# Kernel optimization log

Hardware: AMD Instinct MI355X
Metric: run time of the kernel (lower is better)

## Reference

```python
import jax, jax.numpy as jnp
import numpy as np

SIZE = 64            # size
DIST = 4             # distance (4x4x4 unshared window)
PAD = DIST // 2      # 2
DS = SIZE - 4        # depth of voxel grid (60)
CONVEY = 0.9
RATE = 5
FC_IN = DS * SIZE * SIZE  # (size-4)*size*size = 245760


def setup_inputs() -> dict:
    key = jax.random.key(0)
    ks = jax.random.split(key, 8)
    vinput = jax.random.normal(ks[0], (DS, SIZE, SIZE, 4), dtype=jnp.float32)
    # location-specific (unshared) 4x4x4 synapse weights per voxel
    synapse = jax.random.normal(ks[1], (DS, SIZE, SIZE, DIST, DIST, DIST), dtype=jnp.float32)
    W1 = jax.random.normal(ks[2], (1024, FC_IN), dtype=jnp.float32) / np.float32(np.sqrt(FC_IN))
    b1 = jnp.zeros((1024,), jnp.float32)
    W2 = jax.random.normal(ks[3], (128, 1024), dtype=jnp.float32) / np.float32(np.sqrt(1024))
    b2 = jnp.zeros((128,), jnp.float32)
    W3 = jax.random.normal(ks[4], (10, 128), dtype=jnp.float32) / np.float32(np.sqrt(128))
    b3 = jnp.zeros((10,), jnp.float32)
    return {"vinput": vinput, "synapse": synapse, "W1": W1, "b1": b1,
            "W2": W2, "b2": b2, "W3": W3, "b3": b3}


def _forward(vinput, synapse, W1, b1, W2, b2, W3, b3):
    # frame is zeros, so neuron_matrix = pad(vinput) on the 3 spatial dims
    nm = jnp.pad(vinput, ((PAD, PAD), (PAD, PAD), (PAD, PAD), (0, 0)))  # (DS+2P, S+2P, S+2P, 4)
    ofs = jnp.arange(DIST)
    # gather indices for the 4x4x4 windows anchored at the top-left (as in the source)
    wi = (jnp.arange(DS)[:, None] + ofs)[:, None, None, :, None, None]
    wj = (jnp.arange(SIZE)[:, None] + ofs)[None, :, None, None, :, None]
    wk = (jnp.arange(SIZE)[:, None] + ofs)[None, None, :, None, None, :]
    for _ in range(RATE):
        # synapse (d,d,d) broadcasts over channel, so the full sum factors
        # through the channel-sum of the neuron matrix.
        ns = nm.sum(-1)                       # (DS+2P, S+2P, S+2P)
        win = ns[wi, wj, wk]                  # (DS, S, S, d, d, d)
        core = jnp.einsum('ijkabc,ijkabc->ijk', synapse, win)  # (DS, S, S)
        # dummy is written only at [0:DS, 0:S, 0:S]; border stays zero.
        nm = jnp.zeros_like(nm).at[:DS, :SIZE, :SIZE, :].set(
            (jax.nn.relu(core) * CONVEY)[..., None])
    x = nm[PAD:DS + PAD, PAD:SIZE + PAD, PAD:SIZE + PAD, :]  # (DS, S, S, 4)
    x = x.reshape(-1, FC_IN)                                 # (4, FC_IN), row-major like torch view
    x = jax.nn.relu(x @ W1.T + b1)
    x = jax.nn.relu(x @ W2.T + b2)
    return x @ W3.T + b3                                     # (4, 10)


def reference(vinput, synapse, W1, b1, W2, b2, W3, b3):
    return _forward(vinput, synapse, W1, b1, W2, b2, W3, b3)
```

## Files before the change

### kernel.cpp

```cpp
#include <hip/hip_runtime.h>

#define DSX 60
#define SZ  64
#define NPT (DSX*SZ*SZ)
#define NS_P 64
#define NS_Q 68
#define NS_R 68
#define NS_SZ (NS_P*NS_Q*NS_R)
#define P_PER_ROW 61440
#define KSPLIT 4
#define P_CHUNK (P_PER_ROW / KSPLIT)
#define PB_SLAB (15*NS_Q*NS_R)

typedef float fx4 __attribute__((ext_vector_type(4)));

__global__ __launch_bounds__(256) void fill_pb(const float* __restrict__ vin,
                                               float* __restrict__ PB0,
                                               float* __restrict__ PB1) {
    int t = blockIdx.x * 256 + threadIdx.x;
    if (t >= NS_SZ) return;
    int r = t % NS_R;
    int q = (t / NS_R) % NS_Q;
    int p = t / (NS_R * NS_Q);
    float val = 0.f;
    if (p >= 2 && p < 62 && q >= 2 && q < 66 && r >= 2 && r < 66) {
        const float* b = vin + ((((size_t)(p - 2) * SZ) + (q - 2)) * SZ + (r - 2)) * 4;
        val = (b[0] + b[1]) + (b[2] + b[3]);
    }
    PB0[t] = val;
    PB1[t] = 0.f;
}

__global__ __launch_bounds__(256) void conv_kernel(const float* __restrict__ PBin,
                                                   const float* __restrict__ syn,
                                                   float* __restrict__ PBout) {
    int t = blockIdx.x * 256 + threadIdx.x;
    if (t >= NPT) return;
    int k = t & 63;
    int j = (t >> 6) & 63;
    int i = t >> 12;
    const float4* s4 = (const float4*)syn + (size_t)t * 16;
    float acc = 0.f;
#pragma unroll
    for (int a = 0; a < 4; a++) {
#pragma unroll
        for (int b = 0; b < 4; b++) {
            float4 w = s4[a * 4 + b];
            const float* nrow = PBin + ((size_t)(i + a) * NS_Q + (j + b)) * NS_R + k;
            acc += w.x * nrow[0] + w.y * nrow[1] + w.z * nrow[2] + w.w * nrow[3];
        }
    }
    PBout[((size_t)i * NS_Q + j) * NS_R + k] = acc > 0.f ? acc * 3.6f : 0.f;
}

__global__ __launch_bounds__(256) void gemv1(const float* __restrict__ W1,
                                             const float* __restrict__ PB,
                                             float* __restrict__ partial) {
    int n = blockIdx.x >> 2;
    int c = blockIdx.x & 3;
    const fx4* w4 = (const fx4*)(W1 + (size_t)n * (P_PER_ROW * 4));
    float a0 = 0.f, a1 = 0.f, a2 = 0.f, a3 = 0.f;
#pragma unroll 4
    for (int it = 0; it < P_CHUNK / 256; it++) {
        int p = c * P_CHUNK + it * 256 + threadIdx.x;
        fx4 w = __builtin_nontemporal_load(&w4[p]);
        float s = (w.x + w.y) + (w.z + w.w);
        int iloc = p >> 12;
        int j = (p >> 6) & 63;
        int k = p & 63;
        int base = ((iloc + 2) * NS_Q + (j + 2)) * NS_R + (k + 2);
        a0 += s * PB[base];
        a1 += s * PB[base + PB_SLAB];
        a2 += s * PB[base + 2 * PB_SLAB];
        a3 += s * PB[base + 3 * PB_SLAB];
    }
#pragma unroll
    for (int off = 32; off; off >>= 1) {
        a0 += __shfl_down(a0, off);
        a1 += __shfl_down(a1, off);
        a2 += __shfl_down(a2, off);
        a3 += __shfl_down(a3, off);
    }
    __shared__ float red[4][4];
    int lane = threadIdx.x & 63, wv = threadIdx.x >> 6;
    if (lane == 0) { red[wv][0] = a0; red[wv][1] = a1; red[wv][2] = a2; red[wv][3] = a3; }
    __syncthreads();
    if (threadIdx.x < 4) {
        int r = threadIdx.x;
        float s = (red[0][r] + red[1][r]) + (red[2][r] + red[3][r]);
        partial[((size_t)c * 4 + r) * 1024 + n] = s;
    }
}

__global__ __launch_bounds__(256) void fc2(const float* __restrict__ W2,
                                           const float* __restrict__ b1,
                                           const float* __restrict__ b2,
                                           const float* __restrict__ partial,
                                           float* __restrict__ h2) {
    int n = blockIdx.x;
    float a0 = 0.f, a1 = 0.f, a2 = 0.f, a3 = 0.f;
    for (int e = threadIdx.x; e < 1024; e += 256) {
        float w = W2[(size_t)n * 1024 + e];
        float be = b1[e];
#pragma unroll
        for (int r = 0; r < 4; r++) {
            float h = 0.25f * (partial[(0 * 4 + r) * 1024 + e] + partial[(1 * 4 + r) * 1024 + e] +
                               partial[(2 * 4 + r) * 1024 + e] + partial[(3 * 4 + r) * 1024 + e]) + be;
            h = h > 0.f ? h : 0.f;
            if (r == 0) a0 += w * h;
            else if (r == 1) a1 += w * h;
            else if (r == 2) a2 += w * h;
            else a3 += w * h;
        }
    }
#pragma unroll
    for (int off = 32; off; off >>= 1) {
        a0 += __shfl_down(a0, off);
        a1 += __shfl_down(a1, off);
        a2 += __shfl_down(a2, off);
        a3 += __shfl_down(a3, off);
    }
    __shared__ float red[4][4];
    int lane = threadIdx.x & 63, wv = threadIdx.x >> 6;
    if (lane == 0) { red[wv][0] = a0; red[wv][1] = a1; red[wv][2] = a2; red[wv][3] = a3; }
    __syncthreads();
    if (threadIdx.x < 4) {
        int r = threadIdx.x;
        float s = (red[0][r] + red[1][r]) + (red[2][r] + red[3][r]) + b2[n];
        h2[(size_t)r * 128 + n] = s > 0.f ? s : 0.f;
    }
}

__global__ __launch_bounds__(64) void fc3(const float* __restrict__ W3,
                                          const float* __restrict__ b3,
                                          const float* __restrict__ h2,
                                          float* __restrict__ out) {
    int t = threadIdx.x;
    if (t < 40) {
        int r = t / 10, n = t % 10;
        float a = b3[n];
        for (int e = 0; e < 128; e++) a += W3[(size_t)n * 128 + e] * h2[(size_t)r * 128 + e];
        out[t] = a;
    }
}

extern "C" void kernel_launch(void* const* d_in, const int* in_sizes, int n_in,
                              void* d_out, int out_size, void* d_ws, size_t ws_size,
                              hipStream_t stream) {
    const float* vin = (const float*)d_in[0];
    const float* syn = (const float*)d_in[1];
    const float* W1  = (const float*)d_in[2];
    const float* b1  = (const float*)d_in[3];
    const float* W2  = (const float*)d_in[4];
    const float* b2  = (const float*)d_in[5];
    const float* W3  = (const float*)d_in[6];
    const float* b3  = (const float*)d_in[7];
    float* out = (float*)d_out;

    float* ws = (float*)d_ws;
    float* PB0 = ws;
    float* PB1 = PB0 + NS_SZ;
    float* partial = PB1 + NS_SZ;
    float* h2 = partial + 16 * 1024;

    const int nsBlocks = (NS_SZ + 255) / 256;
    const int ptBlocks = (NPT + 255) / 256;

    fill_pb<<<nsBlocks, 256, 0, stream>>>(vin, PB0, PB1);
    float* cur = PB0; float* nxt = PB1;
    for (int it = 0; it < 5; it++) {
        conv_kernel<<<ptBlocks, 256, 0, stream>>>(cur, syn, nxt);
        float* tmp = cur; cur = nxt; nxt = tmp;
    }
    gemv1<<<1024 * KSPLIT, 256, 0, stream>>>(W1, cur, partial);
    fc2<<<128, 256, 0, stream>>>(W2, b1, b2, partial, h2);
    fc3<<<1, 64, 0, stream>>>(W3, b3, h2, out);
}
```

Baseline: 282.4 us.

## Transpose synapse weights to structure-of-arrays for coalesced conv loads

Adds a kernel that transposes the per-voxel 64-float synapse blocks into 16 planes of float4 indexed by voxel, so adjacent threads in the conv kernel read adjacent float4s. In the old layout each thread read 256 contiguous bytes, which strided the loads across a wavefront on every one of the five iterations. The transpose costs one extra read and write of the whole synapse tensor (about 63 MB) and extra workspace, and it is paid back only if the coalesced loads across five conv passes save more than that. The bounds check in the conv kernel is also dropped because the voxel count divides evenly into blocks.

```diff
diff --git a/kernel.cpp b/kernel.cpp
--- a/kernel.cpp
+++ b/kernel.cpp
@@ -31,24 +31,48 @@
     PB1[t] = 0.f;
 }
 
+__global__ __launch_bounds__(256) void transpose_syn(const float* __restrict__ syn,
+                                                     float* __restrict__ synT) {
+    __shared__ float tile[64 * 65];
+    int t0 = blockIdx.x * 64;
+    const fx4* s4 = (const fx4*)syn;
+#pragma unroll
+    for (int r = 0; r < 4; r++) {
+        int idx = r * 256 + threadIdx.x;
+        int pl = idx >> 4, g = idx & 15;
+        fx4 v = s4[(size_t)(t0 + pl) * 16 + g];
+        int base = pl * 65 + g * 4;
+        tile[base] = v.x; tile[base + 1] = v.y; tile[base + 2] = v.z; tile[base + 3] = v.w;
+    }
+    __syncthreads();
+    int l = threadIdx.x & 63;
+    int wv = threadIdx.x >> 6;
+    fx4* oT = (fx4*)synT;
+#pragma unroll
+    for (int r = 0; r < 4; r++) {
+        int g = r * 4 + wv;
+        int base = l * 65 + g * 4;
+        fx4 v;
+        v.x = tile[base]; v.y = tile[base + 1]; v.z = tile[base + 2]; v.w = tile[base + 3];
+        oT[(size_t)g * NPT + t0 + l] = v;
+    }
+}
+
 __global__ __launch_bounds__(256) void conv_kernel(const float* __restrict__ PBin,
-                                                   const float* __restrict__ syn,
+                                                   const float* __restrict__ synT,
                                                    float* __restrict__ PBout) {
     int t = blockIdx.x * 256 + threadIdx.x;
-    if (t >= NPT) return;
     int k = t & 63;
     int j = (t >> 6) & 63;
     int i = t >> 12;
-    const float4* s4 = (const float4*)syn + (size_t)t * 16;
+    const fx4* sT = (const fx4*)synT;
     float acc = 0.f;
 #pragma unroll
-    for (int a = 0; a < 4; a++) {
-#pragma unroll
-        for (int b = 0; b < 4; b++) {
-            float4 w = s4[a * 4 + b];
-            const float* nrow = PBin + ((size_t)(i + a) * NS_Q + (j + b)) * NS_R + k;
-            acc += w.x * nrow[0] + w.y * nrow[1] + w.z * nrow[2] + w.w * nrow[3];
-        }
+    for (int g = 0; g < 16; g++) {
+        fx4 w = sT[(size_t)g * NPT + t];
+        int a = g >> 2, b = g & 3;
+        const float* nrow = PBin + ((size_t)(i + a) * NS_Q + (j + b)) * NS_R + k;
+        acc += w.x * nrow[0] + w.y * nrow[1] + w.z * nrow[2] + w.w * nrow[3];
     }
     PBout[((size_t)i * NS_Q + j) * NS_R + k] = acc > 0.f ? acc * 3.6f : 0.f;
 }
@@ -162,14 +186,16 @@
     float* PB1 = PB0 + NS_SZ;
     float* partial = PB1 + NS_SZ;
     float* h2 = partial + 16 * 1024;
+    float* synT = h2 + 1024;
 
     const int nsBlocks = (NS_SZ + 255) / 256;
-    const int ptBlocks = (NPT + 255) / 256;
-
+    const int ptBlocks = NPT / 256;
+
+    transpose_syn<<<NPT / 64, 256, 0, stream>>>(syn, synT);
     fill_pb<<<nsBlocks, 256, 0, stream>>>(vin, PB0, PB1);
     float* cur = PB0; float* nxt = PB1;
     for (int it = 0; it < 5; it++) {
-        conv_kernel<<<ptBlocks, 256, 0, stream>>>(cur, syn, nxt);
+        conv_kernel<<<ptBlocks, 256, 0, stream>>>(cur, synT, nxt);
         float* tmp = cur; cur = nxt; nxt = tmp;
     }
     gemv1<<<1024 * KSPLIT, 256, 0, stream>>>(W1, cur, partial);
```

Result: faster. 275.6 us (-2.4%).
